# Performance work log

Measured on AMD Instinct MI355X. Metric: run time of the kernel, lower is better.

The kernel has to match this reference:

```python
import jax, jax.numpy as jnp
import numpy as np

D_MODEL = 2048
N_HEADS = 16
D_HEAD = 128
D_LATENT = 512


def setup_inputs() -> dict:
    key = jax.random.key(0)
    ks = jax.random.split(key, 5)
    s = lambda fan_in: 1.0 / np.sqrt(fan_in)
    x = jax.random.normal(ks[0], (2, 2048, D_MODEL), dtype=jnp.float32)
    # nn.Linear weights stored as [out, in]; we keep [in, out] for x @ W
    W_q = jax.random.uniform(ks[1], (D_MODEL, N_HEADS * D_HEAD), jnp.float32, -s(D_MODEL), s(D_MODEL))
    W_kv_down = jax.random.uniform(ks[2], (D_MODEL, D_LATENT), jnp.float32, -s(D_MODEL), s(D_MODEL))
    W_kv_up = jax.random.uniform(ks[3], (D_LATENT, N_HEADS * D_HEAD), jnp.float32, -s(D_LATENT), s(D_LATENT))
    W_o = jax.random.uniform(ks[4], (N_HEADS * D_HEAD, D_MODEL), jnp.float32, -s(N_HEADS * D_HEAD), s(N_HEADS * D_HEAD))
    return {"x": x, "W_q": W_q, "W_kv_down": W_kv_down, "W_kv_up": W_kv_up, "W_o": W_o}


def reference(x, W_q, W_kv_down, W_kv_up, W_o):
    B, S, _ = x.shape
    # q: [B, H, S, Dh]
    q = (x @ W_q).reshape(B, S, N_HEADS, D_HEAD).transpose(0, 2, 1, 3)
    # latent compression then up-projection; shared K = V
    latent = x @ W_kv_down                      # [B, S, Dl]
    kv = (latent @ W_kv_up).reshape(B, S, N_HEADS, D_HEAD).transpose(0, 2, 1, 3)
    scale = 1.0 / np.sqrt(D_HEAD).astype(np.float32)
    scores = jnp.einsum('bhqd,bhkd->bhqk', q, kv) * scale  # [B,H,S,S]
    probs = jax.nn.softmax(scores, axis=-1)
    out = jnp.einsum('bhqk,bhkd->bhqd', probs, kv)          # [B,H,S,Dh]
    out = out.transpose(0, 2, 1, 3).reshape(B, S, N_HEADS * D_HEAD)
    return out @ W_o
```

## Files before the change

kernel.cpp:

```cpp
#include <hip/hip_runtime.h>

typedef __attribute__((ext_vector_type(8))) __bf16 bf16x8;
typedef __attribute__((ext_vector_type(4))) float f32x4;
typedef __attribute__((ext_vector_type(8))) unsigned short u16x8;
typedef __attribute__((ext_vector_type(4))) unsigned short u16x4;
typedef __attribute__((ext_vector_type(2))) unsigned int u32x2;
typedef __attribute__((ext_vector_type(4))) unsigned int u32x4;

#define MFMA16(a, b, c) __builtin_amdgcn_mfma_f32_16x16x32_bf16((a), (b), (c), 0, 0, 0)

__device__ __forceinline__ unsigned short f2bf(float f) {
    unsigned int u = __float_as_uint(f);
    unsigned int r = (u + 0x7FFFu + ((u >> 16) & 1u)) >> 16;
    return (unsigned short)r;
}

__device__ __forceinline__ float fexp2(float x) {
#if __has_builtin(__builtin_amdgcn_exp2f)
    return __builtin_amdgcn_exp2f(x);
#else
    return exp2f(x);
#endif
}

__device__ __forceinline__ u32x2 plswap32(unsigned int x, unsigned int y) {
#if __has_builtin(__builtin_amdgcn_permlane32_swap)
    return __builtin_amdgcn_permlane32_swap(x, y, false, false);
#else
    asm volatile("s_nop 1\n\tv_permlane32_swap_b32 %0, %1" : "+v"(x), "+v"(y));
    u32x2 r = {x, y};
    return r;
#endif
}
__device__ __forceinline__ u32x2 plswap16(unsigned int x, unsigned int y) {
#if __has_builtin(__builtin_amdgcn_permlane16_swap)
    return __builtin_amdgcn_permlane16_swap(x, y, false, false);
#else
    asm volatile("s_nop 1\n\tv_permlane16_swap_b32 %0, %1" : "+v"(x), "+v"(y));
    u32x2 r = {x, y};
    return r;
#endif
}

__device__ __forceinline__ float quad_reduce(float v) {
    u32x2 a = plswap32(__float_as_uint(v), __float_as_uint(v));
    v = __uint_as_float(a.x) + __uint_as_float(a.y);
    u32x2 b = plswap16(__float_as_uint(v), __float_as_uint(v));
    return __uint_as_float(b.x) + __uint_as_float(b.y);
}

__device__ __forceinline__ void transpose_tile(const float* __restrict__ in,
                                               unsigned short* __restrict__ out,
                                               int R, int C, int bx, int by) {
    __shared__ float tile[32][33];
    const int tx = threadIdx.x & 31, ty = threadIdx.x >> 5;
    const int c0 = bx * 32, r0 = by * 32;
#pragma unroll
    for (int i = 0; i < 4; ++i)
        tile[ty + i * 8][tx] = in[(size_t)(r0 + ty + i * 8) * C + c0 + tx];
    __syncthreads();
#pragma unroll
    for (int i = 0; i < 4; ++i)
        out[(size_t)(c0 + ty + i * 8) * R + r0 + tx] = f2bf(tile[tx][ty + i * 8]);
}

__global__ __launch_bounds__(256) void k_prep(const float* __restrict__ x,
                                              const float* __restrict__ Wq,
                                              const float* __restrict__ Wkvd,
                                              const float* __restrict__ Wkvu,
                                              const float* __restrict__ Wo,
                                              unsigned short* __restrict__ xb,
                                              unsigned short* __restrict__ Wcat_t,
                                              unsigned short* __restrict__ Wkvu_t,
                                              unsigned short* __restrict__ Wo_t) {
    const int i = blockIdx.x;
    if (i < 8192) {
        const int idx = i * 256 + threadIdx.x;
        const float4 v = ((const float4*)x)[idx];
        u16x4 o = { f2bf(v.x), f2bf(v.y), f2bf(v.z), f2bf(v.w) };
        ((u16x4*)xb)[idx] = o;
    } else if (i < 12288) {
        const int j = i - 8192;
        transpose_tile(Wq, Wcat_t, 2048, 2048, j & 63, j >> 6);
    } else if (i < 13312) {
        const int j = i - 12288;
        transpose_tile(Wkvd, Wcat_t + 2048 * 2048, 2048, 512, j & 15, j >> 4);
    } else if (i < 14336) {
        const int j = i - 13312;
        transpose_tile(Wkvu, Wkvu_t, 512, 2048, j & 63, j >> 6);
    } else {
        const int j = i - 14336;
        transpose_tile(Wo, Wo_t, 2048, 2048, j & 63, j >> 6);
    }
}

template <int OUT_MODE>
__global__ __launch_bounds__(256) void k_gemm_bt(const unsigned short* __restrict__ A,
                                                 const unsigned short* __restrict__ B,
                                                 void* __restrict__ Cv,
                                                 unsigned short* __restrict__ Ct,
                                                 int M, int N, int K, float alpha) {
    __shared__ alignas(16) unsigned short As[2 * 128 * 32];
    __shared__ alignas(16) unsigned short Bs[2 * 128 * 32];
    const int tid = threadIdx.x;
    const int wave = tid >> 6;
    const int lane = tid & 63;
    const int l16 = lane & 15;
    const int quad = lane >> 4;
    const int bm = blockIdx.x * 128;
    const int bn = blockIdx.y * 128;
    const int wm = (wave >> 1) * 64;
    const int wn = (wave & 1) * 64;

    const f32x4 fzero = {0.f, 0.f, 0.f, 0.f};
    f32x4 acc[4][4];
#pragma unroll
    for (int i = 0; i < 4; ++i)
#pragma unroll
        for (int j = 0; j < 4; ++j) acc[i][j] = fzero;

    auto AsL = (__attribute__((address_space(3))) unsigned short*)As;
    auto BsL = (__attribute__((address_space(3))) unsigned short*)Bs;

    const int c0 = wave * 128 + lane;

    auto stage = [&](int kt32) {
        const int boff = (kt32 & 1) * (128 * 32);
        const int kt = kt32 * 32;
#pragma unroll
        for (int j = 0; j < 2; ++j) {
            const int c = c0 + j * 64;
            __builtin_amdgcn_global_load_lds(
                (const __attribute__((address_space(1))) void*)(A + (size_t)(bm + (c >> 2)) * K + kt + (c & 3) * 8),
                (__attribute__((address_space(3))) void*)(AsL + boff + c * 8), 16, 0, 0);
            __builtin_amdgcn_global_load_lds(
                (const __attribute__((address_space(1))) void*)(B + (size_t)(bn + (c >> 2)) * K + kt + (c & 3) * 8),
                (__attribute__((address_space(3))) void*)(BsL + boff + c * 8), 16, 0, 0);
        }
    };

    const int nk = K >> 5;
    stage(0);
    for (int kt32 = 0; kt32 < nk; ++kt32) {
        __syncthreads();
        if (kt32 + 1 < nk) stage(kt32 + 1);
        const unsigned short* Ab = As + (kt32 & 1) * (128 * 32);
        const unsigned short* Bb = Bs + (kt32 & 1) * (128 * 32);

        bf16x8 af[4], bfr[4];
#pragma unroll
        for (int mt = 0; mt < 4; ++mt)
            af[mt] = *(const bf16x8*)(Ab + (wm + mt * 16 + l16) * 32 + quad * 8);
#pragma unroll
        for (int nt = 0; nt < 4; ++nt)
            bfr[nt] = *(const bf16x8*)(Bb + (wn + nt * 16 + l16) * 32 + quad * 8);
#pragma unroll
        for (int mt = 0; mt < 4; ++mt)
#pragma unroll
            for (int nt = 0; nt < 4; ++nt)
                acc[mt][nt] = MFMA16(af[mt], bfr[nt], acc[mt][nt]);
    }

#pragma unroll
    for (int mt = 0; mt < 4; ++mt)
#pragma unroll
        for (int nt = 0; nt < 4; ++nt) {
            const int row0 = bm + wm + mt * 16 + quad * 4;
            const int col = bn + wn + nt * 16 + l16;
            u16x4 pk;
#pragma unroll
            for (int r = 0; r < 4; ++r) {
                const float v0 = acc[mt][nt][r];
                if (OUT_MODE == 0) {
                    ((float*)Cv)[(size_t)(row0 + r) * N + col] = v0 * alpha;
                } else if (OUT_MODE == 3) {
                    if (col < 2048)
                        ((unsigned short*)Cv)[(size_t)(row0 + r) * 2048 + col] = f2bf(v0 * alpha);
                    else
                        Ct[(size_t)(row0 + r) * 512 + (col - 2048)] = f2bf(v0);
                } else {
                    const unsigned short b = f2bf(v0 * alpha);
                    ((unsigned short*)Cv)[(size_t)(row0 + r) * N + col] = b;
                    pk[r] = b;
                }
            }
            if (OUT_MODE == 2) {
                const size_t ti =
                    ((size_t)((row0 >> 11) * (N >> 7) + (col >> 7)) * 128 + (col & 127)) * 2048 +
                    (row0 & 2047);
                *(u16x4*)(Ct + ti) = pk;
            }
        }
}

__global__ __launch_bounds__(256, 2) void k_attn(const unsigned short* __restrict__ Q,
                                                 const unsigned short* __restrict__ KV,
                                                 const unsigned short* __restrict__ KVT,
                                                 unsigned short* __restrict__ O) {
    __shared__ alignas(16) unsigned short Ks[2 * 64 * 128];
    __shared__ alignas(16) unsigned short Vt[2 * 128 * 64];

    const int tid = threadIdx.x;
    const int wave = tid >> 6, lane = tid & 63;
    const int l16 = lane & 15, quad = lane >> 4;
    const int l8 = l16 & 7;
    const int lid = blockIdx.x + (blockIdx.y << 4);
    const int wid = ((lid & 7) << 6) + (lid >> 3);
    const int qt = wid & 15;
    const int bh = wid >> 4;
    const size_t tokbase = (size_t)(bh >> 4) * 2048;
    const int hcol = (bh & 15) * 128;
    const unsigned short* kvt_head = KVT + (size_t)bh * (128 * 2048);

    bf16x8 qf[2][4];
    const int qrow0 = qt * 128 + wave * 32;
#pragma unroll
    for (int nt = 0; nt < 2; ++nt) {
        const unsigned short* qp =
            Q + (tokbase + qrow0 + nt * 16 + l16) * 2048 + hcol + quad * 8;
#pragma unroll
        for (int kd = 0; kd < 4; ++kd) qf[nt][kd] = *(const bf16x8*)(qp + kd * 32);
    }

    const f32x4 fzero = {0.f, 0.f, 0.f, 0.f};
    f32x4 o_acc[8][2];
#pragma unroll
    for (int dt = 0; dt < 8; ++dt)
#pragma unroll
        for (int nt = 0; nt < 2; ++nt) o_acc[dt][nt] = fzero;
    float l_i[2] = {0.f, 0.f};

    auto KsL = (__attribute__((address_space(3))) unsigned short*)Ks;
    auto VtL = (__attribute__((address_space(3))) unsigned short*)Vt;

    const int r4 = tid >> 4, cdK = tid & 15;
    const int csK = (cdK & 8) | ((cdK & 7) ^ (r4 & 7));
    const int dv = tid >> 3, cvV = tid & 7;
    const int csV = cvV ^ (dv & 7);
    const unsigned short* kp0 = KV + (tokbase + r4) * 2048 + hcol + csK * 8;
    const unsigned short* vp0 = kvt_head + (size_t)dv * 2048 + csV * 8;

    auto stage = [&](int kt) {
        auto Kb = KsL + (kt & 1) * (64 * 128) + tid * 8;
        auto Vb = VtL + (kt & 1) * (128 * 64) + tid * 8;
        const unsigned short* kp = kp0 + (size_t)kt * (64 * 2048);
        const unsigned short* vp = vp0 + kt * 64;
#pragma unroll
        for (int p = 0; p < 4; ++p) {
            __builtin_amdgcn_global_load_lds(
                (const __attribute__((address_space(1))) void*)(kp + p * (16 * 2048)),
                (__attribute__((address_space(3))) void*)(Kb + p * 2048), 16, 0, 0);
            __builtin_amdgcn_global_load_lds(
                (const __attribute__((address_space(1))) void*)(vp + (size_t)p * (32 * 2048)),
                (__attribute__((address_space(3))) void*)(Vb + p * 2048), 16, 0, 0);
        }
    };

    stage(0);

    for (int kt = 0; kt < 32; ++kt) {
        __syncthreads();
        if (kt < 31) stage(kt + 1);
        const unsigned short* Kb = Ks + (kt & 1) * (64 * 128);
        const unsigned short* Vb = Vt + (kt & 1) * (128 * 64);

        f32x4 st[4][2];
#pragma unroll
        for (int mt = 0; mt < 4; ++mt)
#pragma unroll
            for (int nt = 0; nt < 2; ++nt) st[mt][nt] = fzero;
        __builtin_amdgcn_s_setprio(1);
#pragma unroll
        for (int kd = 0; kd < 4; ++kd)
#pragma unroll
            for (int mt = 0; mt < 4; ++mt) {
                const int c = kd * 4 + quad;
                const int sw = (c & 8) | ((c & 7) ^ l8);
                const bf16x8 kf = *(const bf16x8*)(Kb + (mt * 16 + l16) * 128 + sw * 8);
                st[mt][0] = MFMA16(kf, qf[0][kd], st[mt][0]);
                st[mt][1] = MFMA16(kf, qf[1][kd], st[mt][1]);
            }
        __builtin_amdgcn_s_setprio(0);

        bf16x8 pfr[2][2];
#pragma unroll
        for (int nt = 0; nt < 2; ++nt) {
            float p[4][4];
            float rs = 0.f;
#pragma unroll
            for (int mt = 0; mt < 4; ++mt)
#pragma unroll
                for (int r = 0; r < 4; ++r) {
                    p[mt][r] = fexp2(st[mt][nt][r]);
                    rs += p[mt][r];
                }
            l_i[nt] += rs;
#pragma unroll
            for (int s = 0; s < 2; ++s) {
                unsigned int aw0, aw1, bw0, bw1;
                asm("v_cvt_pk_bf16_f32 %0, %1, %2" : "=v"(aw0) : "v"(p[2 * s][0]), "v"(p[2 * s][1]));
                asm("v_cvt_pk_bf16_f32 %0, %1, %2" : "=v"(aw1) : "v"(p[2 * s][2]), "v"(p[2 * s][3]));
                asm("v_cvt_pk_bf16_f32 %0, %1, %2" : "=v"(bw0) : "v"(p[2 * s + 1][0]), "v"(p[2 * s + 1][1]));
                asm("v_cvt_pk_bf16_f32 %0, %1, %2" : "=v"(bw1) : "v"(p[2 * s + 1][2]), "v"(p[2 * s + 1][3]));
                const u32x2 e0 = plswap32(aw0, bw0);
                const u32x2 e1 = plswap32(aw1, bw1);
                const u32x2 f0 = plswap16(e0.x, e0.y);
                const u32x2 f1 = plswap16(e1.x, e1.y);
                const u32x4 w = {f0.x, f1.x, f0.y, f1.y};
                pfr[s][nt] = __builtin_bit_cast(bf16x8, w);
            }
        }

        __builtin_amdgcn_s_setprio(1);
#pragma unroll
        for (int s = 0; s < 2; ++s) {
            const int sw = ((s * 4 + quad) ^ l8) * 8;
            bf16x8 vf[8];
#pragma unroll
            for (int dt = 0; dt < 8; ++dt)
                vf[dt] = *(const bf16x8*)(Vb + (dt * 16 + l16) * 64 + sw);
#pragma unroll
            for (int dt = 0; dt < 8; ++dt) {
                o_acc[dt][0] = MFMA16(vf[dt], pfr[s][0], o_acc[dt][0]);
                o_acc[dt][1] = MFMA16(vf[dt], pfr[s][1], o_acc[dt][1]);
            }
        }
        __builtin_amdgcn_s_setprio(0);
    }

#pragma unroll
    for (int nt = 0; nt < 2; ++nt) {
        const float inv = 1.0f / quad_reduce(l_i[nt]);
        unsigned short* dst = O + (tokbase + qrow0 + nt * 16 + l16) * 2048 + hcol;
#pragma unroll
        for (int dt = 0; dt < 8; ++dt) {
            u16x4 pk;
#pragma unroll
            for (int r = 0; r < 4; ++r) pk[r] = f2bf(o_acc[dt][nt][r] * inv);
            *(u16x4*)(dst + dt * 16 + quad * 4) = pk;
        }
    }
}

extern "C" void kernel_launch(void* const* d_in, const int* in_sizes, int n_in,
                              void* d_out, int out_size, void* d_ws, size_t ws_size,
                              hipStream_t stream) {
    const float* x = (const float*)d_in[0];
    const float* W_q = (const float*)d_in[1];
    const float* W_kvd = (const float*)d_in[2];
    const float* W_kvu = (const float*)d_in[3];
    const float* W_o = (const float*)d_in[4];

    char* w = (char*)d_ws;
    unsigned short* xb = (unsigned short*)(w);
    unsigned short* kvT = xb;
    unsigned short* qb = (unsigned short*)(w + (size_t)16 * 1024 * 1024);
    unsigned short* kvb = (unsigned short*)(w + (size_t)32 * 1024 * 1024);
    unsigned short* Wo_t = (unsigned short*)(w + (size_t)48 * 1024 * 1024);
    unsigned short* Wcat_t = (unsigned short*)(w + (size_t)56 * 1024 * 1024);
    unsigned short* Wkvu_t = (unsigned short*)(w + (size_t)66 * 1024 * 1024);
    unsigned short* lat = (unsigned short*)(w + (size_t)68 * 1024 * 1024);

    k_prep<<<18432, 256, 0, stream>>>(x, W_q, W_kvd, W_kvu, W_o, xb, Wcat_t, Wkvu_t, Wo_t);

    k_gemm_bt<3><<<dim3(32, 20), 256, 0, stream>>>(xb, Wcat_t, qb, lat, 4096, 2560, 2048,
                                                   0.12751743f);
    k_gemm_bt<2><<<dim3(32, 16), 256, 0, stream>>>(lat, Wkvu_t, kvb, kvT, 4096, 2048, 512,
                                                   1.0f);
    k_attn<<<dim3(16, 32), 256, 0, stream>>>(qb, kvb, kvT, qb);
    k_gemm_bt<0><<<dim3(32, 16), 256, 0, stream>>>(qb, Wo_t, d_out, nullptr, 4096, 2048, 2048,
                                                   1.0f);
}
```

Baseline: 306.4 us.

## Software-pipeline attention loop with 32-key tiles and four-stage LDS ring

Splits each 64-key tile into two 32-key tiles held in a four-buffer LDS ring, prefetching two tiles ahead. The loop is restructured so the QK^T MFMAs for tile k are issued together with the PV MFMAs for tile k-1, while softmax (exp and bf16 pack) for the next tile runs afterwards. The goal is to overlap exp/VALU work with matrix-core work and hide global-to-LDS latency. In exchange it doubles the number of barriers per key span and changes the V swizzle, with some added code complexity and register pressure.

```diff
diff --git a/kernel.cpp b/kernel.cpp
--- a/kernel.cpp
+++ b/kernel.cpp
@@ -197,8 +197,8 @@
                                                  const unsigned short* __restrict__ KV,
                                                  const unsigned short* __restrict__ KVT,
                                                  unsigned short* __restrict__ O) {
-    __shared__ alignas(16) unsigned short Ks[2 * 64 * 128];
-    __shared__ alignas(16) unsigned short Vt[2 * 128 * 64];
+    __shared__ alignas(16) unsigned short Ks[4 * 32 * 128];
+    __shared__ alignas(16) unsigned short Vt[4 * 128 * 32];
 
     const int tid = threadIdx.x;
     const int wave = tid >> 6, lane = tid & 63;
@@ -235,98 +235,121 @@
 
     const int r4 = tid >> 4, cdK = tid & 15;
     const int csK = (cdK & 8) | ((cdK & 7) ^ (r4 & 7));
-    const int dv = tid >> 3, cvV = tid & 7;
-    const int csV = cvV ^ (dv & 7);
+    const int dv = tid >> 2, cvV = tid & 3;
+    const int csV = cvV ^ ((tid >> 3) & 3);
     const unsigned short* kp0 = KV + (tokbase + r4) * 2048 + hcol + csK * 8;
     const unsigned short* vp0 = kvt_head + (size_t)dv * 2048 + csV * 8;
 
     auto stage = [&](int kt) {
-        auto Kb = KsL + (kt & 1) * (64 * 128) + tid * 8;
-        auto Vb = VtL + (kt & 1) * (128 * 64) + tid * 8;
-        const unsigned short* kp = kp0 + (size_t)kt * (64 * 2048);
-        const unsigned short* vp = vp0 + kt * 64;
-#pragma unroll
-        for (int p = 0; p < 4; ++p) {
+        auto Kb = KsL + (kt & 3) * (32 * 128) + tid * 8;
+        auto Vb = VtL + (kt & 3) * (128 * 32) + tid * 8;
+        const unsigned short* kp = kp0 + (size_t)kt * (32 * 2048);
+        const unsigned short* vp = vp0 + kt * 32;
+#pragma unroll
+        for (int p = 0; p < 2; ++p) {
             __builtin_amdgcn_global_load_lds(
                 (const __attribute__((address_space(1))) void*)(kp + p * (16 * 2048)),
                 (__attribute__((address_space(3))) void*)(Kb + p * 2048), 16, 0, 0);
             __builtin_amdgcn_global_load_lds(
-                (const __attribute__((address_space(1))) void*)(vp + (size_t)p * (32 * 2048)),
+                (const __attribute__((address_space(1))) void*)(vp + (size_t)p * (64 * 2048)),
                 (__attribute__((address_space(3))) void*)(Vb + p * 2048), 16, 0, 0);
         }
     };
 
-    stage(0);
-
-    for (int kt = 0; kt < 32; ++kt) {
-        __syncthreads();
-        if (kt < 31) stage(kt + 1);
-        const unsigned short* Kb = Ks + (kt & 1) * (64 * 128);
-        const unsigned short* Vb = Vt + (kt & 1) * (128 * 64);
-
-        f32x4 st[4][2];
-#pragma unroll
-        for (int mt = 0; mt < 4; ++mt)
+    const int vsw = (quad ^ ((l16 >> 1) & 3)) * 8;
+
+    f32x4 st[2][2];
+    auto qk = [&](int kt) {
+        const unsigned short* Kb = Ks + (kt & 3) * (32 * 128);
+#pragma unroll
+        for (int mt = 0; mt < 2; ++mt)
 #pragma unroll
             for (int nt = 0; nt < 2; ++nt) st[mt][nt] = fzero;
-        __builtin_amdgcn_s_setprio(1);
 #pragma unroll
         for (int kd = 0; kd < 4; ++kd)
 #pragma unroll
-            for (int mt = 0; mt < 4; ++mt) {
+            for (int mt = 0; mt < 2; ++mt) {
                 const int c = kd * 4 + quad;
                 const int sw = (c & 8) | ((c & 7) ^ l8);
                 const bf16x8 kf = *(const bf16x8*)(Kb + (mt * 16 + l16) * 128 + sw * 8);
                 st[mt][0] = MFMA16(kf, qf[0][kd], st[mt][0]);
                 st[mt][1] = MFMA16(kf, qf[1][kd], st[mt][1]);
             }
-        __builtin_amdgcn_s_setprio(0);
-
-        bf16x8 pfr[2][2];
+    };
+    auto pv = [&](int kt, bf16x8 (&pfr)[2]) {
+        const unsigned short* Vb = Vt + (kt & 3) * (128 * 32);
+#pragma unroll
+        for (int dt = 0; dt < 8; ++dt) {
+            const bf16x8 vf = *(const bf16x8*)(Vb + (dt * 16 + l16) * 32 + vsw);
+            o_acc[dt][0] = MFMA16(vf, pfr[0], o_acc[dt][0]);
+            o_acc[dt][1] = MFMA16(vf, pfr[1], o_acc[dt][1]);
+        }
+    };
+    auto sm = [&](bf16x8 (&pfr)[2]) {
 #pragma unroll
         for (int nt = 0; nt < 2; ++nt) {
-            float p[4][4];
+            float p[2][4];
             float rs = 0.f;
 #pragma unroll
-            for (int mt = 0; mt < 4; ++mt)
+            for (int mt = 0; mt < 2; ++mt)
 #pragma unroll
                 for (int r = 0; r < 4; ++r) {
                     p[mt][r] = fexp2(st[mt][nt][r]);
                     rs += p[mt][r];
                 }
             l_i[nt] += rs;
-#pragma unroll
-            for (int s = 0; s < 2; ++s) {
-                unsigned int aw0, aw1, bw0, bw1;
-                asm("v_cvt_pk_bf16_f32 %0, %1, %2" : "=v"(aw0) : "v"(p[2 * s][0]), "v"(p[2 * s][1]));
-                asm("v_cvt_pk_bf16_f32 %0, %1, %2" : "=v"(aw1) : "v"(p[2 * s][2]), "v"(p[2 * s][3]));
-                asm("v_cvt_pk_bf16_f32 %0, %1, %2" : "=v"(bw0) : "v"(p[2 * s + 1][0]), "v"(p[2 * s + 1][1]));
-                asm("v_cvt_pk_bf16_f32 %0, %1, %2" : "=v"(bw1) : "v"(p[2 * s + 1][2]), "v"(p[2 * s + 1][3]));
-                const u32x2 e0 = plswap32(aw0, bw0);
-                const u32x2 e1 = plswap32(aw1, bw1);
-                const u32x2 f0 = plswap16(e0.x, e0.y);
-                const u32x2 f1 = plswap16(e1.x, e1.y);
-                const u32x4 w = {f0.x, f1.x, f0.y, f1.y};
-                pfr[s][nt] = __builtin_bit_cast(bf16x8, w);
-            }
-        }
-
+            unsigned int aw0, aw1, bw0, bw1;
+            asm("v_cvt_pk_bf16_f32 %0, %1, %2" : "=v"(aw0) : "v"(p[0][0]), "v"(p[0][1]));
+            asm("v_cvt_pk_bf16_f32 %0, %1, %2" : "=v"(aw1) : "v"(p[0][2]), "v"(p[0][3]));
+            asm("v_cvt_pk_bf16_f32 %0, %1, %2" : "=v"(bw0) : "v"(p[1][0]), "v"(p[1][1]));
+            asm("v_cvt_pk_bf16_f32 %0, %1, %2" : "=v"(bw1) : "v"(p[1][2]), "v"(p[1][3]));
+            const u32x2 e0 = plswap32(aw0, bw0);
+            const u32x2 e1 = plswap32(aw1, bw1);
+            const u32x2 f0 = plswap16(e0.x, e0.y);
+            const u32x2 f1 = plswap16(e1.x, e1.y);
+            const u32x4 w = {f0.x, f1.x, f0.y, f1.y};
+            pfr[nt] = __builtin_bit_cast(bf16x8, w);
+        }
+    };
+
+    bf16x8 pfrA[2], pfrB[2];
+
+    stage(0);
+    stage(1);
+    __syncthreads();
+    stage(2);
+    __builtin_amdgcn_s_setprio(1);
+    qk(0);
+    __builtin_amdgcn_s_setprio(0);
+    sm(pfrA);
+
+    for (int kt2 = 1; kt2 <= 31; ++kt2) {
+        const int ko = 2 * kt2 - 1;
+        __syncthreads();
+        stage(ko + 2);
         __builtin_amdgcn_s_setprio(1);
-#pragma unroll
-        for (int s = 0; s < 2; ++s) {
-            const int sw = ((s * 4 + quad) ^ l8) * 8;
-            bf16x8 vf[8];
-#pragma unroll
-            for (int dt = 0; dt < 8; ++dt)
-                vf[dt] = *(const bf16x8*)(Vb + (dt * 16 + l16) * 64 + sw);
-#pragma unroll
-            for (int dt = 0; dt < 8; ++dt) {
-                o_acc[dt][0] = MFMA16(vf[dt], pfr[s][0], o_acc[dt][0]);
-                o_acc[dt][1] = MFMA16(vf[dt], pfr[s][1], o_acc[dt][1]);
-            }
-        }
+        qk(ko);
+        pv(ko - 1, pfrA);
         __builtin_amdgcn_s_setprio(0);
-    }
+        sm(pfrB);
+
+        const int ke = 2 * kt2;
+        __syncthreads();
+        if (ke < 62) stage(ke + 2);
+        __builtin_amdgcn_s_setprio(1);
+        qk(ke);
+        pv(ke - 1, pfrB);
+        __builtin_amdgcn_s_setprio(0);
+        sm(pfrA);
+    }
+
+    __syncthreads();
+    __builtin_amdgcn_s_setprio(1);
+    qk(63);
+    pv(62, pfrA);
+    __builtin_amdgcn_s_setprio(0);
+    sm(pfrB);
+    pv(63, pfrB);
 
 #pragma unroll
     for (int nt = 0; nt < 2; ++nt) {
```

After: 312.4 us. No clear change (+2.0%).

## Switch attention kernel from 16x16x32 to 32x32x16 MFMA tiles

Applied to the files above, without the earlier changes.

Rewrites the attention kernel's QK^T and PV matrix products to use 32x32x16 bf16 MFMA instead of 16x16x32, with each wave covering 32 query rows as a single 32-wide tile. Fragment layouts, the probability repacking (now one permlane32 swap instead of two swaps), the row-sum reduction and the output store pattern all change to match. The larger MFMA tile means fewer LDS fragment loads per FLOP and fewer instructions issued. In exchange it uses larger accumulator vectors and may change register pressure and latency hiding.

```diff
diff --git a/kernel.cpp b/kernel.cpp
--- a/kernel.cpp
+++ b/kernel.cpp
@@ -2,12 +2,14 @@
 
 typedef __attribute__((ext_vector_type(8))) __bf16 bf16x8;
 typedef __attribute__((ext_vector_type(4))) float f32x4;
+typedef __attribute__((ext_vector_type(16))) float f32x16;
 typedef __attribute__((ext_vector_type(8))) unsigned short u16x8;
 typedef __attribute__((ext_vector_type(4))) unsigned short u16x4;
 typedef __attribute__((ext_vector_type(2))) unsigned int u32x2;
 typedef __attribute__((ext_vector_type(4))) unsigned int u32x4;
 
 #define MFMA16(a, b, c) __builtin_amdgcn_mfma_f32_16x16x32_bf16((a), (b), (c), 0, 0, 0)
+#define MFMA32(a, b, c) __builtin_amdgcn_mfma_f32_32x32x16_bf16((a), (b), (c), 0, 0, 0)
 
 __device__ __forceinline__ unsigned short f2bf(float f) {
     unsigned int u = __float_as_uint(f);
@@ -202,8 +204,9 @@
 
     const int tid = threadIdx.x;
     const int wave = tid >> 6, lane = tid & 63;
-    const int l16 = lane & 15, quad = lane >> 4;
-    const int l8 = l16 & 7;
+    const int q31 = lane & 31;
+    const int hi = lane >> 5;
+    const int l8 = q31 & 7;
     const int lid = blockIdx.x + (blockIdx.y << 4);
     const int wid = ((lid & 7) << 6) + (lid >> 3);
     const int qt = wid & 15;
@@ -212,23 +215,20 @@
     const int hcol = (bh & 15) * 128;
     const unsigned short* kvt_head = KVT + (size_t)bh * (128 * 2048);
 
-    bf16x8 qf[2][4];
+    bf16x8 qf[8];
     const int qrow0 = qt * 128 + wave * 32;
-#pragma unroll
-    for (int nt = 0; nt < 2; ++nt) {
-        const unsigned short* qp =
-            Q + (tokbase + qrow0 + nt * 16 + l16) * 2048 + hcol + quad * 8;
-#pragma unroll
-        for (int kd = 0; kd < 4; ++kd) qf[nt][kd] = *(const bf16x8*)(qp + kd * 32);
-    }
-
-    const f32x4 fzero = {0.f, 0.f, 0.f, 0.f};
-    f32x4 o_acc[8][2];
-#pragma unroll
-    for (int dt = 0; dt < 8; ++dt)
-#pragma unroll
-        for (int nt = 0; nt < 2; ++nt) o_acc[dt][nt] = fzero;
-    float l_i[2] = {0.f, 0.f};
+    {
+        const unsigned short* qp = Q + (tokbase + qrow0 + q31) * 2048 + hcol + hi * 8;
+#pragma unroll
+        for (int kd = 0; kd < 8; ++kd) qf[kd] = *(const bf16x8*)(qp + kd * 16);
+    }
+
+    f32x16 o_acc[4];
+#pragma unroll
+    for (int dt = 0; dt < 4; ++dt)
+#pragma unroll
+        for (int r = 0; r < 16; ++r) o_acc[dt][r] = 0.f;
+    float l_i = 0.f;
 
     auto KsL = (__attribute__((address_space(3))) unsigned short*)Ks;
     auto VtL = (__attribute__((address_space(3))) unsigned short*)Vt;
@@ -264,81 +264,74 @@
         const unsigned short* Kb = Ks + (kt & 1) * (64 * 128);
         const unsigned short* Vb = Vt + (kt & 1) * (128 * 64);
 
-        f32x4 st[4][2];
-#pragma unroll
-        for (int mt = 0; mt < 4; ++mt)
-#pragma unroll
-            for (int nt = 0; nt < 2; ++nt) st[mt][nt] = fzero;
+        f32x16 st[2];
+#pragma unroll
+        for (int r = 0; r < 16; ++r) { st[0][r] = 0.f; st[1][r] = 0.f; }
         __builtin_amdgcn_s_setprio(1);
 #pragma unroll
-        for (int kd = 0; kd < 4; ++kd)
-#pragma unroll
-            for (int mt = 0; mt < 4; ++mt) {
-                const int c = kd * 4 + quad;
-                const int sw = (c & 8) | ((c & 7) ^ l8);
-                const bf16x8 kf = *(const bf16x8*)(Kb + (mt * 16 + l16) * 128 + sw * 8);
-                st[mt][0] = MFMA16(kf, qf[0][kd], st[mt][0]);
-                st[mt][1] = MFMA16(kf, qf[1][kd], st[mt][1]);
-            }
+        for (int kd = 0; kd < 8; ++kd) {
+            const int c = 2 * kd + hi;
+            const int sw = (c & 8) | ((c & 7) ^ l8);
+#pragma unroll
+            for (int mt = 0; mt < 2; ++mt) {
+                const bf16x8 kf = *(const bf16x8*)(Kb + (mt * 32 + q31) * 128 + sw * 8);
+                st[mt] = MFMA32(kf, qf[kd], st[mt]);
+            }
+        }
         __builtin_amdgcn_s_setprio(0);
 
-        bf16x8 pfr[2][2];
-#pragma unroll
-        for (int nt = 0; nt < 2; ++nt) {
-            float p[4][4];
+        bf16x8 pfrk[2][2];
+#pragma unroll
+        for (int mt = 0; mt < 2; ++mt) {
+            float p[16];
             float rs = 0.f;
 #pragma unroll
-            for (int mt = 0; mt < 4; ++mt)
-#pragma unroll
-                for (int r = 0; r < 4; ++r) {
-                    p[mt][r] = fexp2(st[mt][nt][r]);
-                    rs += p[mt][r];
-                }
-            l_i[nt] += rs;
+            for (int r = 0; r < 16; ++r) {
+                p[r] = fexp2(st[mt][r]);
+                rs += p[r];
+            }
+            l_i += rs;
 #pragma unroll
             for (int s = 0; s < 2; ++s) {
-                unsigned int aw0, aw1, bw0, bw1;
-                asm("v_cvt_pk_bf16_f32 %0, %1, %2" : "=v"(aw0) : "v"(p[2 * s][0]), "v"(p[2 * s][1]));
-                asm("v_cvt_pk_bf16_f32 %0, %1, %2" : "=v"(aw1) : "v"(p[2 * s][2]), "v"(p[2 * s][3]));
-                asm("v_cvt_pk_bf16_f32 %0, %1, %2" : "=v"(bw0) : "v"(p[2 * s + 1][0]), "v"(p[2 * s + 1][1]));
-                asm("v_cvt_pk_bf16_f32 %0, %1, %2" : "=v"(bw1) : "v"(p[2 * s + 1][2]), "v"(p[2 * s + 1][3]));
-                const u32x2 e0 = plswap32(aw0, bw0);
-                const u32x2 e1 = plswap32(aw1, bw1);
-                const u32x2 f0 = plswap16(e0.x, e0.y);
-                const u32x2 f1 = plswap16(e1.x, e1.y);
-                const u32x4 w = {f0.x, f1.x, f0.y, f1.y};
-                pfr[s][nt] = __builtin_bit_cast(bf16x8, w);
+                unsigned int w0, w1, w2, w3;
+                asm("v_cvt_pk_bf16_f32 %0, %1, %2" : "=v"(w0) : "v"(p[s * 8 + 0]), "v"(p[s * 8 + 1]));
+                asm("v_cvt_pk_bf16_f32 %0, %1, %2" : "=v"(w1) : "v"(p[s * 8 + 2]), "v"(p[s * 8 + 3]));
+                asm("v_cvt_pk_bf16_f32 %0, %1, %2" : "=v"(w2) : "v"(p[s * 8 + 4]), "v"(p[s * 8 + 5]));
+                asm("v_cvt_pk_bf16_f32 %0, %1, %2" : "=v"(w3) : "v"(p[s * 8 + 6]), "v"(p[s * 8 + 7]));
+                const u32x2 u02 = plswap32(w0, w2);
+                const u32x2 u13 = plswap32(w1, w3);
+                const u32x4 w = {u02.x, u13.x, u02.y, u13.y};
+                pfrk[mt][s] = __builtin_bit_cast(bf16x8, w);
             }
         }
 
         __builtin_amdgcn_s_setprio(1);
 #pragma unroll
-        for (int s = 0; s < 2; ++s) {
-            const int sw = ((s * 4 + quad) ^ l8) * 8;
-            bf16x8 vf[8];
-#pragma unroll
-            for (int dt = 0; dt < 8; ++dt)
-                vf[dt] = *(const bf16x8*)(Vb + (dt * 16 + l16) * 64 + sw);
-#pragma unroll
-            for (int dt = 0; dt < 8; ++dt) {
-                o_acc[dt][0] = MFMA16(vf[dt], pfr[s][0], o_acc[dt][0]);
-                o_acc[dt][1] = MFMA16(vf[dt], pfr[s][1], o_acc[dt][1]);
+        for (int ks = 0; ks < 4; ++ks) {
+            const int swv = ((2 * ks + hi) ^ l8) * 8;
+            const bf16x8 pf = pfrk[ks >> 1][ks & 1];
+#pragma unroll
+            for (int dt = 0; dt < 4; ++dt) {
+                const bf16x8 vf = *(const bf16x8*)(Vb + (dt * 32 + q31) * 64 + swv);
+                o_acc[dt] = MFMA32(vf, pf, o_acc[dt]);
             }
         }
         __builtin_amdgcn_s_setprio(0);
     }
 
-#pragma unroll
-    for (int nt = 0; nt < 2; ++nt) {
-        const float inv = 1.0f / quad_reduce(l_i[nt]);
-        unsigned short* dst = O + (tokbase + qrow0 + nt * 16 + l16) * 2048 + hcol;
-#pragma unroll
-        for (int dt = 0; dt < 8; ++dt) {
-            u16x4 pk;
-#pragma unroll
-            for (int r = 0; r < 4; ++r) pk[r] = f2bf(o_acc[dt][nt][r] * inv);
-            *(u16x4*)(dst + dt * 16 + quad * 4) = pk;
-        }
+    {
+        const u32x2 a = plswap32(__float_as_uint(l_i), __float_as_uint(l_i));
+        const float inv = 1.0f / (__uint_as_float(a.x) + __uint_as_float(a.y));
+        unsigned short* dst = O + (tokbase + qrow0 + q31) * 2048 + hcol + hi * 4;
+#pragma unroll
+        for (int dt = 0; dt < 4; ++dt)
+#pragma unroll
+            for (int g = 0; g < 4; ++g) {
+                u16x4 pk;
+#pragma unroll
+                for (int j = 0; j < 4; ++j) pk[j] = f2bf(o_acc[dt][g * 4 + j] * inv);
+                *(u16x4*)(dst + dt * 32 + g * 8) = pk;
+            }
     }
 }
 
```

Measured after the change: 309.9 us. About the same (+1.2%).
